# Performance work log

Hardware: AMD Instinct MI355X
Metric: run time of the kernel (lower is better)

The kernel has to match this reference:

```python
import jax, jax.numpy as jnp
import numpy as np
import math

B, D_MODEL, H, D_K, L = 24, 128, 8, 16, 512


def setup_inputs() -> dict:
    key = jax.random.key(0)
    ks = jax.random.split(key, 5)
    x = jax.random.normal(ks[0], (B, D_MODEL, L), dtype=jnp.float32)
    Wq = jax.random.normal(ks[1], (H, B, D_K, D_MODEL), dtype=jnp.float32)
    Wk = jax.random.normal(ks[2], (H, B, D_K, D_MODEL), dtype=jnp.float32)
    Wv = jax.random.normal(ks[3], (H, B, D_K, D_MODEL), dtype=jnp.float32)
    Wo = jax.random.normal(ks[4], (B, H * D_K, D_MODEL), dtype=jnp.float32)
    return {"x": x, "Wq": Wq, "Wk": Wk, "Wv": Wv, "Wo": Wo}


def reference(x, Wq, Wk, Wv, Wo):
    # Per-head, per-batch projections: [h,b,k,d] @ [b,d,l] -> [h,b,k,l]
    Q = jnp.einsum('hbkd,bdl->hbkl', Wq, x)
    K = jnp.einsum('hbkd,bdl->hbkl', Wk, x)
    V = jnp.einsum('hbkd,bdl->hbkl', Wv, x)
    # scores[h,b,l,m] = Q[:, :, :, l] . K[:, :, :, m]; torch softmax dim=1 of
    # the [B, L, L] score -> softmax over the QUERY axis l (axis=2 here).
    scores = jnp.einsum('hbkl,hbkm->hblm', Q, K) / math.sqrt(D_K)
    attn = jax.nn.softmax(scores, axis=2)
    # head_i = V @ attn : [h,b,v,l] @ [h,b,l,m] -> [h,b,v,m]
    heads = jnp.einsum('hbvl,hblm->hbvm', V, attn)
    # concat heads along channel dim: [b, h*v, L]
    head = heads.transpose(1, 0, 2, 3).reshape(B, H * D_K, L)
    # out = Wo @ head : [b, h*v, d_model] treated as [b,128,128] @ [b,128,L]
    out = jnp.einsum('bod,bdl->bol', Wo, head)
    return out
```

## Files before the change

kernel.cpp:

```cpp
#include <hip/hip_runtime.h>
#include <math.h>

#define NB 24
#define DM 128
#define NH 8
#define DK 16
#define LL 512
#define HB (NH * NB)

#define XTH_OFF 0
#define XTL_OFF 3145728
#define HT_OFF  6291456

typedef __attribute__((ext_vector_type(8))) short bf16x8;
typedef __attribute__((ext_vector_type(4))) float f32x4;
typedef __attribute__((ext_vector_type(4))) int   i32x4;

#define MFMA  __builtin_amdgcn_mfma_f32_16x16x32_bf16
#define EXP2  __builtin_amdgcn_exp2f
#define BPERM __builtin_amdgcn_ds_bpermute

static __device__ __forceinline__ unsigned bfr(float x) {
    return (__float_as_uint(x) + 0x8000u) & 0xffff0000u;
}

static __device__ __forceinline__ unsigned cvtpk(float a, float b) {
    unsigned r;
    asm("v_cvt_pk_bf16_f32 %0, %1, %2" : "=v"(r) : "v"(a), "v"(b));
    return r;
}

static __device__ __forceinline__ void wsplit(const float* __restrict__ p,
                                              bf16x8& aH, bf16x8& aL) {
    const float4 f0 = *(const float4*)p;
    const float4 f1 = *(const float4*)(p + 4);
    const float f[8] = {f0.x, f0.y, f0.z, f0.w, f1.x, f1.y, f1.z, f1.w};
    i32x4 h, l;
    #pragma unroll
    for (int q = 0; q < 4; ++q) {
        const unsigned h0 = bfr(f[2 * q]), h1 = bfr(f[2 * q + 1]);
        const unsigned e0 = bfr(f[2 * q]     - __uint_as_float(h0));
        const unsigned e1 = bfr(f[2 * q + 1] - __uint_as_float(h1));
        h[q] = (int)((h0 >> 16) | (h1 & 0xffff0000u));
        l[q] = (int)((e0 >> 16) | (e1 & 0xffff0000u));
    }
    aH = __builtin_bit_cast(bf16x8, h);
    aL = __builtin_bit_cast(bf16x8, l);
}

__global__ __launch_bounds__(256)
void prep(const float* __restrict__ x,
          unsigned short* __restrict__ xthi,
          unsigned short* __restrict__ xtlo)
{
    __shared__ float T[64][65];
    const int bid = blockIdx.x, tid = threadIdx.x;
    const int b = bid >> 3, lc = bid & 7;

    #pragma unroll
    for (int half = 0; half < 2; ++half) {
        const int d0 = half << 6;
        const float* __restrict__ xb =
            x + (size_t)b * 65536 + (size_t)d0 * LL + lc * 64;
        if (half) __syncthreads();
        #pragma unroll
        for (int i = 0; i < 16; ++i) {
            const int idx = i * 256 + tid;
            T[idx >> 6][idx & 63] = xb[(size_t)(idx >> 6) * LL + (idx & 63)];
        }
        __syncthreads();
        #pragma unroll
        for (int i = 0; i < 8; ++i) {
            const int idx = (i * 256 + tid) * 2;
            const int l = idx >> 6, dd = idx & 63;
            const float v0 = T[dd][l], v1 = T[dd + 1][l];
            const unsigned h0 = bfr(v0), h1 = bfr(v1);
            const unsigned e0 = bfr(v0 - __uint_as_float(h0));
            const unsigned e1 = bfr(v1 - __uint_as_float(h1));
            const size_t o = (size_t)b * 65536 +
                             (size_t)(lc * 64 + l) * DM + d0 + dd;
            *(unsigned*)(xthi + o) = (h0 >> 16) | (h1 & 0xffff0000u);
            *(unsigned*)(xtlo + o) = (e0 >> 16) | (e1 & 0xffff0000u);
        }
    }
}

static __device__ __forceinline__ void soft_pv(
    const f32x4& s0, const f32x4& s1, float tm, float& bar, float& sm,
    f32x4& O, const bf16x8& aV, int aLo, int aHi, bool up)
{
    const float nb = fmaxf(bar, tm + 32.f);
    const float f  = EXP2(bar - nb);
    bar = nb;
    const float e0 = EXP2(s0[0] - nb), e1 = EXP2(s0[1] - nb);
    const float e2 = EXP2(s0[2] - nb), e3 = EXP2(s0[3] - nb);
    const float e4 = EXP2(s1[0] - nb), e5 = EXP2(s1[1] - nb);
    const float e6 = EXP2(s1[2] - nb), e7 = EXP2(s1[3] - nb);
    const float sacc = ((e0 + e1) + (e2 + e3)) + ((e4 + e5) + (e6 + e7));
    sm = fmaf(sm, f, sacc);
    O *= f;
    const unsigned c0 = cvtpk(e0, e1), c1 = cvtpk(e2, e3);
    const unsigned c2 = cvtpk(e4, e5), c3 = cvtpk(e6, e7);
    const int p00 = BPERM(aLo, (int)c0), p02 = BPERM(aLo, (int)c2);
    const int p10 = BPERM(aLo, (int)c1), p12 = BPERM(aLo, (int)c3);
    const int p20 = BPERM(aHi, (int)c0), p22 = BPERM(aHi, (int)c2);
    const int p30 = BPERM(aHi, (int)c1), p32 = BPERM(aHi, (int)c3);
    i32x4 bi = { up ? p00 : p02, up ? p10 : p12,
                 up ? p20 : p22, up ? p30 : p32 };
    O = MFMA(aV, __builtin_bit_cast(bf16x8, bi), O, 0, 0, 0);
}

#define QK_STRIDE 40
#define V_STRIDE  520

__global__ __launch_bounds__(1024)
void qkv_attn(const unsigned short* __restrict__ xthi,
              const unsigned short* __restrict__ xtlo,
              const float* __restrict__ Wq,
              const float* __restrict__ Wk,
              const float* __restrict__ Wv,
              unsigned short* __restrict__ ht)
{
    __shared__ unsigned short qs[LL * QK_STRIDE];
    __shared__ unsigned short ks[LL * QK_STRIDE];
    __shared__ unsigned short vs[DK * V_STRIDE];

    const int hb    = blockIdx.x;
    const int b     = hb % NB;
    const int wv    = threadIdx.x >> 6;
    const int lane  = threadIdx.x & 63;
    const int g     = lane >> 4;
    const int mR    = lane & 15;
    const int lQ    = wv * 32;

    {
        const float* __restrict__ wqp = Wq + (size_t)hb * 2048 + mR * 128 + g * 8;
        const float* __restrict__ wkp = Wk + (size_t)hb * 2048 + mR * 128 + g * 8;
        const float* __restrict__ wvp = Wv + (size_t)hb * 2048 + mR * 128 + g * 8;
        const unsigned short* __restrict__ xh = xthi + (size_t)b * 65536 + g * 8;
        const unsigned short* __restrict__ xl = xtlo + (size_t)b * 65536 + g * 8;

        f32x4 CQ[2], CK[2], CV[2];
        #pragma unroll
        for (int t = 0; t < 2; ++t) {
            CQ[t] = (f32x4){0.f, 0.f, 0.f, 0.f};
            CK[t] = (f32x4){0.f, 0.f, 0.f, 0.f};
            CV[t] = (f32x4){0.f, 0.f, 0.f, 0.f};
        }

        #pragma unroll
        for (int kk = 0; kk < 4; ++kk) {
            bf16x8 bH[2], bL[2];
            #pragma unroll
            for (int t = 0; t < 2; ++t) {
                const size_t ro = (size_t)(lQ + t * 16 + mR) * DM + kk * 32;
                bH[t] = *(const bf16x8*)(xh + ro);
                bL[t] = *(const bf16x8*)(xl + ro);
            }
            bf16x8 aH, aL;
            wsplit(wqp + kk * 32, aH, aL);
            #pragma unroll
            for (int t = 0; t < 2; ++t) {
                CQ[t] = MFMA(aH, bH[t], CQ[t], 0, 0, 0);
                CQ[t] = MFMA(aH, bL[t], CQ[t], 0, 0, 0);
                CQ[t] = MFMA(aL, bH[t], CQ[t], 0, 0, 0);
            }
            wsplit(wkp + kk * 32, aH, aL);
            #pragma unroll
            for (int t = 0; t < 2; ++t) {
                CK[t] = MFMA(aH, bH[t], CK[t], 0, 0, 0);
                CK[t] = MFMA(aH, bL[t], CK[t], 0, 0, 0);
                CK[t] = MFMA(aL, bH[t], CK[t], 0, 0, 0);
            }
            wsplit(wvp + kk * 32, aH, aL);
            #pragma unroll
            for (int t = 0; t < 2; ++t) {
                CV[t] = MFMA(aH, bH[t], CV[t], 0, 0, 0);
                CV[t] = MFMA(aH, bL[t], CV[t], 0, 0, 0);
                CV[t] = MFMA(aL, bH[t], CV[t], 0, 0, 0);
            }
        }

        #pragma unroll
        for (int t = 0; t < 2; ++t) {
            const int l = lQ + t * 16 + mR;
            #pragma unroll
            for (int i = 0; i < 4; ++i)
                vs[(4 * g + i) * V_STRIDE + l] =
                    (unsigned short)(bfr(CV[t][i]) >> 16);
        }
        #pragma unroll
        for (int t = 0; t < 2; ++t) {
            const int l = lQ + t * 16 + mR;
            ushort4 hi4, lo4;
            #pragma unroll
            for (int i = 0; i < 4; ++i) {
                const float v = CQ[t][i];
                const unsigned h = bfr(v);
                const unsigned lw = bfr(v - __uint_as_float(h));
                ((unsigned short*)&hi4)[i] = (unsigned short)(h >> 16);
                ((unsigned short*)&lo4)[i] = (unsigned short)(lw >> 16);
            }
            *(ushort4*)(qs + l * QK_STRIDE + 4 * g)      = hi4;
            *(ushort4*)(qs + l * QK_STRIDE + 16 + 4 * g) = lo4;
        }
        #pragma unroll
        for (int t = 0; t < 2; ++t) {
            const int r = lQ + t * 16 + mR;
            ushort4 hi4, lo4;
            #pragma unroll
            for (int i = 0; i < 4; ++i) {
                const float v = CK[t][i] * (0.25f * 1.44269504f);
                const unsigned h = bfr(v);
                const unsigned lw = bfr(v - __uint_as_float(h));
                ((unsigned short*)&hi4)[i] = (unsigned short)(h >> 16);
                ((unsigned short*)&lo4)[i] = (unsigned short)(lw >> 16);
            }
            *(ushort4*)(ks + r * QK_STRIDE + 4 * g)      = hi4;
            *(ushort4*)(ks + r * QK_STRIDE + 16 + 4 * g) = lo4;
        }
    }

    __syncthreads();

    const int kloc = wv * 32;
    const unsigned short* Kr0 = ks + (kloc + mR) * QK_STRIDE;
    const unsigned short* Kr1 = Kr0 + 16 * QK_STRIDE;
    const bf16x8 K0  = *(const bf16x8*)(Kr0 + g * 8);
    const bf16x8 K0s = *(const bf16x8*)(Kr0 + (g ^ 2) * 8);
    const bf16x8 K1  = *(const bf16x8*)(Kr1 + g * 8);
    const bf16x8 K1s = *(const bf16x8*)(Kr1 + (g ^ 2) * 8);

    const unsigned short* qrow = qs + mR * QK_STRIDE + g * 8;
    const unsigned short* vrow = vs + mR * V_STRIDE + g * 8;

    f32x4 O0 = {0.f,0.f,0.f,0.f}, O1 = {0.f,0.f,0.f,0.f};
    float bar0 = -1e30f, bar1 = -1e30f, sm0 = 0.f, sm1 = 0.f;

    const int aLo = ((g & 1) * 32 + mR) * 4;
    const int aHi = aLo + 64;
    const bool up = (g < 2);

    for (int l = 0; l < LL; l += 32) {
        const bf16x8 aQ0 = *(const bf16x8*)(qrow + l * QK_STRIDE);
        const bf16x8 aQ1 = *(const bf16x8*)(qrow + (l + 16) * QK_STRIDE);
        const bf16x8 aV  = *(const bf16x8*)(vrow + l);

        const f32x4 z = {0.f,0.f,0.f,0.f};
        f32x4 sA0 = MFMA(aQ0, K0, z, 0,0,0);   sA0 = MFMA(aQ0, K0s, sA0, 0,0,0);
        f32x4 sB0 = MFMA(aQ0, K1, z, 0,0,0);   sB0 = MFMA(aQ0, K1s, sB0, 0,0,0);
        f32x4 sA1 = MFMA(aQ1, K0, z, 0,0,0);   sA1 = MFMA(aQ1, K0s, sA1, 0,0,0);
        f32x4 sB1 = MFMA(aQ1, K1, z, 0,0,0);   sB1 = MFMA(aQ1, K1s, sB1, 0,0,0);

        float tmA = fmaxf(fmaxf(fmaxf(sA0[0],sA0[1]), fmaxf(sA0[2],sA0[3])),
                          fmaxf(fmaxf(sA1[0],sA1[1]), fmaxf(sA1[2],sA1[3])));
        float tmB = fmaxf(fmaxf(fmaxf(sB0[0],sB0[1]), fmaxf(sB0[2],sB0[3])),
                          fmaxf(fmaxf(sB1[0],sB1[1]), fmaxf(sB1[2],sB1[3])));
        tmA = fmaxf(tmA, __shfl_xor(tmA, 16, 64));
        tmA = fmaxf(tmA, __shfl_xor(tmA, 32, 64));
        tmB = fmaxf(tmB, __shfl_xor(tmB, 16, 64));
        tmB = fmaxf(tmB, __shfl_xor(tmB, 32, 64));

        const bool pA = __any(tmA + 64.f > bar0);
        const bool pB = __any(tmB + 64.f > bar1);
        if (pA) soft_pv(sA0, sA1, tmA, bar0, sm0, O0, aV, aLo, aHi, up);
        if (pB) soft_pv(sB0, sB1, tmB, bar1, sm1, O1, aV, aLo, aHi, up);
    }

    sm0 += __shfl_xor(sm0, 16, 64);  sm0 += __shfl_xor(sm0, 32, 64);
    sm1 += __shfl_xor(sm1, 16, 64);  sm1 += __shfl_xor(sm1, 32, 64);
    const float i0 = 1.f / sm0, i1 = 1.f / sm1;

    const int h = hb / NB, bb = hb % NB;
    unsigned short* __restrict__ ho =
        ht + (size_t)bb * 65536 + (size_t)(kloc + mR) * DM + h * 16 + 4 * g;
    ushort4 p0, p1;
    #pragma unroll
    for (int i = 0; i < 4; ++i) {
        ((unsigned short*)&p0)[i] = (unsigned short)(bfr(O0[i] * i0) >> 16);
        ((unsigned short*)&p1)[i] = (unsigned short)(bfr(O1[i] * i1) >> 16);
    }
    *(ushort4*)ho             = p0;
    *(ushort4*)(ho + 16 * DM) = p1;
}

__global__ __launch_bounds__(256)
void out_mfma(const float* __restrict__ Wo,
              const unsigned short* __restrict__ ht,
              float* __restrict__ out)
{
    const int blk  = blockIdx.x;
    const int b    = blk >> 5;
    const int mq   = (blk >> 4) & 1;
    const int nq   = blk & 15;
    const int wv   = threadIdx.x >> 6;
    const int lane = threadIdx.x & 63;
    const int g = lane >> 4, mR = lane & 15;
    const int m0 = (mq * 4 + wv) * 16;
    const int n0 = nq * 32;

    const float* __restrict__ A =
        Wo + (size_t)b * 16384 + (size_t)(m0 + mR) * DM + g * 8;
    const unsigned short* __restrict__ B = ht + (size_t)b * 65536 + g * 8;

    f32x4 C0 = {0.f,0.f,0.f,0.f}, C1 = {0.f,0.f,0.f,0.f};
    #pragma unroll
    for (int kk = 0; kk < 4; ++kk) {
        const float4 f0 = *(const float4*)(A + kk * 32);
        const float4 f1 = *(const float4*)(A + kk * 32 + 4);
        i32x4 w;
        w[0] = (int)cvtpk(f0.x, f0.y);
        w[1] = (int)cvtpk(f0.z, f0.w);
        w[2] = (int)cvtpk(f1.x, f1.y);
        w[3] = (int)cvtpk(f1.z, f1.w);
        const bf16x8 aW = __builtin_bit_cast(bf16x8, w);
        const bf16x8 b0 = *(const bf16x8*)(B + (size_t)(n0 + mR) * DM + kk * 32);
        const bf16x8 b1 = *(const bf16x8*)(B + (size_t)(n0 + 16 + mR) * DM + kk * 32);
        C0 = MFMA(aW, b0, C0, 0, 0, 0);
        C1 = MFMA(aW, b1, C1, 0, 0, 0);
    }

    float* __restrict__ ob = out + (size_t)b * 65536 + (size_t)(m0 + 4 * g) * LL;
    #pragma unroll
    for (int i = 0; i < 4; ++i) {
        ob[(size_t)i * LL + n0 + mR]      = C0[i];
        ob[(size_t)i * LL + n0 + 16 + mR] = C1[i];
    }
}

extern "C" void kernel_launch(void* const* d_in, const int* in_sizes, int n_in,
                              void* d_out, int out_size, void* d_ws, size_t ws_size,
                              hipStream_t stream) {
    const float* x  = (const float*)d_in[0];
    const float* Wq = (const float*)d_in[1];
    const float* Wk = (const float*)d_in[2];
    const float* Wv = (const float*)d_in[3];
    const float* Wo = (const float*)d_in[4];
    float* out = (float*)d_out;

    char* ws = (char*)d_ws;
    unsigned short* xthi = (unsigned short*)(ws + XTH_OFF);
    unsigned short* xtlo = (unsigned short*)(ws + XTL_OFF);
    unsigned short* ht   = (unsigned short*)(ws + HT_OFF);

    prep     <<<192,     256,  0, stream>>>(x, xthi, xtlo);
    qkv_attn <<<HB,      1024, 0, stream>>>(xthi, xtlo, Wq, Wk, Wv, ht);
    out_mfma <<<NB * 32, 256,  0, stream>>>(Wo, ht, out);
}
```

Before: 117.0 us.

## Halve attention block size, give each wave 64 columns, and cut bpermutes

```diff
diff --git a/kernel.cpp b/kernel.cpp
--- a/kernel.cpp
+++ b/kernel.cpp
@@ -87,7 +87,7 @@
 
 static __device__ __forceinline__ void soft_pv(
     const f32x4& s0, const f32x4& s1, float tm, float& bar, float& sm,
-    f32x4& O, const bf16x8& aV, int aLo, int aHi, bool up)
+    f32x4& O, const bf16x8& aV, int addr0, int addr1, bool up, bool odd16)
 {
     const float nb = fmaxf(bar, tm + 32.f);
     const float f  = EXP2(bar - nb);
@@ -101,19 +101,23 @@
     O *= f;
     const unsigned c0 = cvtpk(e0, e1), c1 = cvtpk(e2, e3);
     const unsigned c2 = cvtpk(e4, e5), c3 = cvtpk(e6, e7);
-    const int p00 = BPERM(aLo, (int)c0), p02 = BPERM(aLo, (int)c2);
-    const int p10 = BPERM(aLo, (int)c1), p12 = BPERM(aLo, (int)c3);
-    const int p20 = BPERM(aHi, (int)c0), p22 = BPERM(aHi, (int)c2);
-    const int p30 = BPERM(aHi, (int)c1), p32 = BPERM(aHi, (int)c3);
-    i32x4 bi = { up ? p00 : p02, up ? p10 : p12,
-                 up ? p20 : p22, up ? p30 : p32 };
+    const int r0 = (int)(odd16 ? c2 : c0);
+    const int r1 = (int)(odd16 ? c0 : c2);
+    const int r2 = (int)(odd16 ? c3 : c1);
+    const int r3 = (int)(odd16 ? c1 : c3);
+    const int w0 = BPERM(addr0, r0);
+    const int w1 = BPERM(addr1, r1);
+    const int w2 = BPERM(addr0, r2);
+    const int w3 = BPERM(addr1, r3);
+    i32x4 bi = { up ? w0 : w1, up ? w2 : w3,
+                 up ? w1 : w0, up ? w3 : w2 };
     O = MFMA(aV, __builtin_bit_cast(bf16x8, bi), O, 0, 0, 0);
 }
 
 #define QK_STRIDE 40
 #define V_STRIDE  520
 
-__global__ __launch_bounds__(1024)
+__global__ __launch_bounds__(512)
 void qkv_attn(const unsigned short* __restrict__ xthi,
               const unsigned short* __restrict__ xtlo,
               const float* __restrict__ Wq,
@@ -131,7 +135,7 @@
     const int lane  = threadIdx.x & 63;
     const int g     = lane >> 4;
     const int mR    = lane & 15;
-    const int lQ    = wv * 32;
+    const int lQ    = wv * 64;
 
     {
         const float* __restrict__ wqp = Wq + (size_t)hb * 2048 + mR * 128 + g * 8;
@@ -140,9 +144,9 @@
         const unsigned short* __restrict__ xh = xthi + (size_t)b * 65536 + g * 8;
         const unsigned short* __restrict__ xl = xtlo + (size_t)b * 65536 + g * 8;
 
-        f32x4 CQ[2], CK[2], CV[2];
-        #pragma unroll
-        for (int t = 0; t < 2; ++t) {
+        f32x4 CQ[4], CK[4], CV[4];
+        #pragma unroll
+        for (int t = 0; t < 4; ++t) {
             CQ[t] = (f32x4){0.f, 0.f, 0.f, 0.f};
             CK[t] = (f32x4){0.f, 0.f, 0.f, 0.f};
             CV[t] = (f32x4){0.f, 0.f, 0.f, 0.f};
@@ -150,9 +154,9 @@
 
         #pragma unroll
         for (int kk = 0; kk < 4; ++kk) {
-            bf16x8 bH[2], bL[2];
-            #pragma unroll
-            for (int t = 0; t < 2; ++t) {
+            bf16x8 bH[4], bL[4];
+            #pragma unroll
+            for (int t = 0; t < 4; ++t) {
                 const size_t ro = (size_t)(lQ + t * 16 + mR) * DM + kk * 32;
                 bH[t] = *(const bf16x8*)(xh + ro);
                 bL[t] = *(const bf16x8*)(xl + ro);
@@ -160,21 +164,21 @@
             bf16x8 aH, aL;
             wsplit(wqp + kk * 32, aH, aL);
             #pragma unroll
-            for (int t = 0; t < 2; ++t) {
+            for (int t = 0; t < 4; ++t) {
                 CQ[t] = MFMA(aH, bH[t], CQ[t], 0, 0, 0);
                 CQ[t] = MFMA(aH, bL[t], CQ[t], 0, 0, 0);
                 CQ[t] = MFMA(aL, bH[t], CQ[t], 0, 0, 0);
             }
             wsplit(wkp + kk * 32, aH, aL);
             #pragma unroll
-            for (int t = 0; t < 2; ++t) {
+            for (int t = 0; t < 4; ++t) {
                 CK[t] = MFMA(aH, bH[t], CK[t], 0, 0, 0);
                 CK[t] = MFMA(aH, bL[t], CK[t], 0, 0, 0);
                 CK[t] = MFMA(aL, bH[t], CK[t], 0, 0, 0);
             }
             wsplit(wvp + kk * 32, aH, aL);
             #pragma unroll
-            for (int t = 0; t < 2; ++t) {
+            for (int t = 0; t < 4; ++t) {
                 CV[t] = MFMA(aH, bH[t], CV[t], 0, 0, 0);
                 CV[t] = MFMA(aH, bL[t], CV[t], 0, 0, 0);
                 CV[t] = MFMA(aL, bH[t], CV[t], 0, 0, 0);
@@ -182,7 +186,7 @@
         }
 
         #pragma unroll
-        for (int t = 0; t < 2; ++t) {
+        for (int t = 0; t < 4; ++t) {
             const int l = lQ + t * 16 + mR;
             #pragma unroll
             for (int i = 0; i < 4; ++i)
@@ -190,7 +194,7 @@
                     (unsigned short)(bfr(CV[t][i]) >> 16);
         }
         #pragma unroll
-        for (int t = 0; t < 2; ++t) {
+        for (int t = 0; t < 4; ++t) {
             const int l = lQ + t * 16 + mR;
             ushort4 hi4, lo4;
             #pragma unroll
@@ -205,7 +209,7 @@
             *(ushort4*)(qs + l * QK_STRIDE + 16 + 4 * g) = lo4;
         }
         #pragma unroll
-        for (int t = 0; t < 2; ++t) {
+        for (int t = 0; t < 4; ++t) {
             const int r = lQ + t * 16 + mR;
             ushort4 hi4, lo4;
             #pragma unroll
@@ -223,65 +227,95 @@
 
     __syncthreads();
 
-    const int kloc = wv * 32;
-    const unsigned short* Kr0 = ks + (kloc + mR) * QK_STRIDE;
-    const unsigned short* Kr1 = Kr0 + 16 * QK_STRIDE;
-    const bf16x8 K0  = *(const bf16x8*)(Kr0 + g * 8);
-    const bf16x8 K0s = *(const bf16x8*)(Kr0 + (g ^ 2) * 8);
-    const bf16x8 K1  = *(const bf16x8*)(Kr1 + g * 8);
-    const bf16x8 K1s = *(const bf16x8*)(Kr1 + (g ^ 2) * 8);
+    bf16x8 K0[2], K0s[2], K1[2], K1s[2];
+    #pragma unroll
+    for (int sub = 0; sub < 2; ++sub) {
+        const unsigned short* Kr0 = ks + (lQ + sub * 32 + mR) * QK_STRIDE;
+        const unsigned short* Kr1 = Kr0 + 16 * QK_STRIDE;
+        K0[sub]  = *(const bf16x8*)(Kr0 + g * 8);
+        K0s[sub] = *(const bf16x8*)(Kr0 + (g ^ 2) * 8);
+        K1[sub]  = *(const bf16x8*)(Kr1 + g * 8);
+        K1s[sub] = *(const bf16x8*)(Kr1 + (g ^ 2) * 8);
+    }
 
     const unsigned short* qrow = qs + mR * QK_STRIDE + g * 8;
     const unsigned short* vrow = vs + mR * V_STRIDE + g * 8;
 
-    f32x4 O0 = {0.f,0.f,0.f,0.f}, O1 = {0.f,0.f,0.f,0.f};
-    float bar0 = -1e30f, bar1 = -1e30f, sm0 = 0.f, sm1 = 0.f;
-
-    const int aLo = ((g & 1) * 32 + mR) * 4;
-    const int aHi = aLo + 64;
-    const bool up = (g < 2);
+    f32x4 O[2][2];
+    float bar[2][2], sm[2][2];
+    #pragma unroll
+    for (int sub = 0; sub < 2; ++sub)
+        #pragma unroll
+        for (int gr = 0; gr < 2; ++gr) {
+            O[sub][gr]   = (f32x4){0.f, 0.f, 0.f, 0.f};
+            bar[sub][gr] = -1e30f;
+            sm[sub][gr]  = 0.f;
+        }
+
+    const int  aLo   = ((g & 1) * 32 + mR) * 4;
+    const int  aHi   = aLo + 64;
+    const bool up    = (g < 2);
+    const bool odd16 = (g & 1);
+    const int  addr0 = up ? aLo : aHi;
+    const int  addr1 = up ? aHi : aLo;
 
     for (int l = 0; l < LL; l += 32) {
         const bf16x8 aQ0 = *(const bf16x8*)(qrow + l * QK_STRIDE);
         const bf16x8 aQ1 = *(const bf16x8*)(qrow + (l + 16) * QK_STRIDE);
         const bf16x8 aV  = *(const bf16x8*)(vrow + l);
 
-        const f32x4 z = {0.f,0.f,0.f,0.f};
-        f32x4 sA0 = MFMA(aQ0, K0, z, 0,0,0);   sA0 = MFMA(aQ0, K0s, sA0, 0,0,0);
-        f32x4 sB0 = MFMA(aQ0, K1, z, 0,0,0);   sB0 = MFMA(aQ0, K1s, sB0, 0,0,0);
-        f32x4 sA1 = MFMA(aQ1, K0, z, 0,0,0);   sA1 = MFMA(aQ1, K0s, sA1, 0,0,0);
-        f32x4 sB1 = MFMA(aQ1, K1, z, 0,0,0);   sB1 = MFMA(aQ1, K1s, sB1, 0,0,0);
-
-        float tmA = fmaxf(fmaxf(fmaxf(sA0[0],sA0[1]), fmaxf(sA0[2],sA0[3])),
-                          fmaxf(fmaxf(sA1[0],sA1[1]), fmaxf(sA1[2],sA1[3])));
-        float tmB = fmaxf(fmaxf(fmaxf(sB0[0],sB0[1]), fmaxf(sB0[2],sB0[3])),
-                          fmaxf(fmaxf(sB1[0],sB1[1]), fmaxf(sB1[2],sB1[3])));
-        tmA = fmaxf(tmA, __shfl_xor(tmA, 16, 64));
-        tmA = fmaxf(tmA, __shfl_xor(tmA, 32, 64));
-        tmB = fmaxf(tmB, __shfl_xor(tmB, 16, 64));
-        tmB = fmaxf(tmB, __shfl_xor(tmB, 32, 64));
-
-        const bool pA = __any(tmA + 64.f > bar0);
-        const bool pB = __any(tmB + 64.f > bar1);
-        if (pA) soft_pv(sA0, sA1, tmA, bar0, sm0, O0, aV, aLo, aHi, up);
-        if (pB) soft_pv(sB0, sB1, tmB, bar1, sm1, O1, aV, aLo, aHi, up);
-    }
-
-    sm0 += __shfl_xor(sm0, 16, 64);  sm0 += __shfl_xor(sm0, 32, 64);
-    sm1 += __shfl_xor(sm1, 16, 64);  sm1 += __shfl_xor(sm1, 32, 64);
-    const float i0 = 1.f / sm0, i1 = 1.f / sm1;
+        #pragma unroll
+        for (int sub = 0; sub < 2; ++sub) {
+            const f32x4 z = {0.f,0.f,0.f,0.f};
+            f32x4 sA0 = MFMA(aQ0, K0[sub], z, 0,0,0);
+            sA0 = MFMA(aQ0, K0s[sub], sA0, 0,0,0);
+            f32x4 sB0 = MFMA(aQ0, K1[sub], z, 0,0,0);
+            sB0 = MFMA(aQ0, K1s[sub], sB0, 0,0,0);
+            f32x4 sA1 = MFMA(aQ1, K0[sub], z, 0,0,0);
+            sA1 = MFMA(aQ1, K0s[sub], sA1, 0,0,0);
+            f32x4 sB1 = MFMA(aQ1, K1[sub], z, 0,0,0);
+            sB1 = MFMA(aQ1, K1s[sub], sB1, 0,0,0);
+
+            float tmA = fmaxf(fmaxf(fmaxf(sA0[0],sA0[1]), fmaxf(sA0[2],sA0[3])),
+                              fmaxf(fmaxf(sA1[0],sA1[1]), fmaxf(sA1[2],sA1[3])));
+            float tmB = fmaxf(fmaxf(fmaxf(sB0[0],sB0[1]), fmaxf(sB0[2],sB0[3])),
+                              fmaxf(fmaxf(sB1[0],sB1[1]), fmaxf(sB1[2],sB1[3])));
+            tmA = fmaxf(tmA, __shfl_xor(tmA, 16, 64));
+            tmA = fmaxf(tmA, __shfl_xor(tmA, 32, 64));
+            tmB = fmaxf(tmB, __shfl_xor(tmB, 16, 64));
+            tmB = fmaxf(tmB, __shfl_xor(tmB, 32, 64));
+
+            const bool pA = __any(tmA + 64.f > bar[sub][0]);
+            const bool pB = __any(tmB + 64.f > bar[sub][1]);
+            if (pA) soft_pv(sA0, sA1, tmA, bar[sub][0], sm[sub][0],
+                            O[sub][0], aV, addr0, addr1, up, odd16);
+            if (pB) soft_pv(sB0, sB1, tmB, bar[sub][1], sm[sub][1],
+                            O[sub][1], aV, addr0, addr1, up, odd16);
+        }
+    }
 
     const int h = hb / NB, bb = hb % NB;
-    unsigned short* __restrict__ ho =
-        ht + (size_t)bb * 65536 + (size_t)(kloc + mR) * DM + h * 16 + 4 * g;
-    ushort4 p0, p1;
-    #pragma unroll
-    for (int i = 0; i < 4; ++i) {
-        ((unsigned short*)&p0)[i] = (unsigned short)(bfr(O0[i] * i0) >> 16);
-        ((unsigned short*)&p1)[i] = (unsigned short)(bfr(O1[i] * i1) >> 16);
-    }
-    *(ushort4*)ho             = p0;
-    *(ushort4*)(ho + 16 * DM) = p1;
+    #pragma unroll
+    for (int sub = 0; sub < 2; ++sub) {
+        float s0 = sm[sub][0], s1 = sm[sub][1];
+        s0 += __shfl_xor(s0, 16, 64);  s0 += __shfl_xor(s0, 32, 64);
+        s1 += __shfl_xor(s1, 16, 64);  s1 += __shfl_xor(s1, 32, 64);
+        const float i0 = 1.f / s0, i1 = 1.f / s1;
+
+        unsigned short* __restrict__ ho =
+            ht + (size_t)bb * 65536 +
+            (size_t)(lQ + sub * 32 + mR) * DM + h * 16 + 4 * g;
+        ushort4 p0, p1;
+        #pragma unroll
+        for (int i = 0; i < 4; ++i) {
+            ((unsigned short*)&p0)[i] =
+                (unsigned short)(bfr(O[sub][0][i] * i0) >> 16);
+            ((unsigned short*)&p1)[i] =
+                (unsigned short)(bfr(O[sub][1][i] * i1) >> 16);
+        }
+        *(ushort4*)ho             = p0;
+        *(ushort4*)(ho + 16 * DM) = p1;
+    }
 }
 
 __global__ __launch_bounds__(256)
@@ -343,7 +377,7 @@
     unsigned short* xtlo = (unsigned short*)(ws + XTL_OFF);
     unsigned short* ht   = (unsigned short*)(ws + HT_OFF);
 
-    prep     <<<192,     256,  0, stream>>>(x, xthi, xtlo);
-    qkv_attn <<<HB,      1024, 0, stream>>>(xthi, xtlo, Wq, Wk, Wv, ht);
-    out_mfma <<<NB * 32, 256,  0, stream>>>(Wo, ht, out);
-}
+    prep     <<<192,     256, 0, stream>>>(x, xthi, xtlo);
+    qkv_attn <<<HB,      512, 0, stream>>>(xthi, xtlo, Wq, Wk, Wv, ht);
+    out_mfma <<<NB * 32, 256, 0, stream>>>(Wo, ht, out);
+}
```

Result: faster. 113.2 us (-3.2%).
